# Kernel tuning notes

Hardware: AMD Instinct MI355X
Metric: run time of the kernel (lower is better)

The kernel has to match this reference:

```python
import jax, jax.numpy as jnp
import numpy as np

# static config (matches init_kwargs)
B, HID, NH, D = 1, 1024, 16, 64
T, Hh, W = 8, 32, 32
TT, TH, TW = 2, 8, 8            # tile sizes (numel 128)
WT, WH, WW = 6 // TT, 16 // TH, 16 // TW  # window in tiles: 3,2,2
NTT, NTH, NTW = T // TT, Hh // TH, W // TW  # 4,4,4
NTILE = NTT * NTH * NTW          # 64
TILE = TT * TH * TW              # 128
WK = WT * WH * WW                # 12 kv tiles per q tile
S = T * Hh * W


def _dim_window(nt, w):
    left = w // 2
    right = w // 2 + (w % 2) - 1
    center = jnp.clip(jnp.arange(nt), left, nt - 1 - right)
    return center[:, None] - left + jnp.arange(w)  # [nt, w]


def _kv_tile_idx():
    kt = _dim_window(NTT, WT)  # [NTT, WT]
    kh = _dim_window(NTH, WH)  # [NTH, WH]
    kw = _dim_window(NTW, WW)  # [NTW, WW]
    idx = (kt[:, None, None, :, None, None] * (NTH * NTW)
           + kh[None, :, None, None, :, None] * NTW
           + kw[None, None, :, None, None, :])
    return idx.reshape(NTILE, WK)


def _to_tiles(x, nh):
    # [B, S, nh*D] -> [B, nh, NTILE, TILE, D]; seq laid out (ntt tt nth th ntw tw)
    x = x.reshape(B, NTT, TT, NTH, TH, NTW, TW, nh, D)
    x = x.transpose(0, 7, 1, 3, 5, 2, 4, 6, 8)
    return x.reshape(B, nh, NTILE, TILE, D)


def _from_tiles(o):
    # [B, NH, NTILE, TILE, D] -> [B, S, NH*D]
    o = o.reshape(B, NH, NTT, NTH, NTW, TT, TH, TW, D)
    o = o.transpose(0, 2, 5, 3, 6, 4, 7, 1, 8)
    return o.reshape(B, S, NH * D)


def setup_inputs() -> dict:
    key = jax.random.key(0)
    ks = jax.random.split(key, 5)
    sc = 1.0 / np.sqrt(HID)
    return {
        'hidden_states': jax.random.normal(ks[0], (B, S, HID), jnp.float32),
        'wq': jax.random.normal(ks[1], (HID, NH * D), jnp.float32) * sc,
        'wk': jax.random.normal(ks[2], (HID, NH * D), jnp.float32) * sc,
        'wv': jax.random.normal(ks[3], (HID, NH * D), jnp.float32) * sc,
        'wo': jax.random.normal(ks[4], (NH * D, HID), jnp.float32) * sc,
    }


def reference(hidden_states, wq, wk, wv, wo):
    kv_idx = _kv_tile_idx()  # [NTILE, WK]
    q = _to_tiles(hidden_states @ wq, NH)  # [B,NH,NTILE,TILE,D]
    k = _to_tiles(hidden_states @ wk, NH)
    v = _to_tiles(hidden_states @ wv, NH)
    # gather each query tile's exact kv window (mask fully satisfied by construction)
    kg = k[:, :, kv_idx].reshape(B, NH, NTILE, WK * TILE, D)
    vg = v[:, :, kv_idx].reshape(B, NH, NTILE, WK * TILE, D)
    scores = jnp.einsum('bhnqd,bhnkd->bhnqk', q, kg) * (1.0 / np.sqrt(D))
    p = jax.nn.softmax(scores, axis=-1)
    o = jnp.einsum('bhnqk,bhnkd->bhnqd', p, vg)
    return _from_tiles(o) @ wo
```

## Files before the change

kernel.cpp:

```cpp
#include <hip/hip_runtime.h>
#include <hip/hip_bf16.h>
#include <math.h>

typedef __attribute__((ext_vector_type(8))) short          short8;
typedef __attribute__((ext_vector_type(8))) unsigned short u16x8;
typedef __attribute__((ext_vector_type(2))) unsigned int   u32x2;
typedef __attribute__((ext_vector_type(4))) float          f32x4;

#define MFMA_BF16(a, b, c) __builtin_amdgcn_mfma_f32_16x16x32_bf16((a), (b), (c), 0, 0, 0)

#define GLOAD_LDS16(gp, lp)                                        \
  __builtin_amdgcn_global_load_lds(                                \
      (const __attribute__((address_space(1))) void*)(gp),         \
      (__attribute__((address_space(3))) void*)(lp), 16, 0, 0)


__device__ __forceinline__ unsigned short f2bf(float f) {
  union { float f; unsigned int u; } v; v.f = f;
  unsigned int r = v.u + 0x7fffu + ((v.u >> 16) & 1u);
  return (unsigned short)(r >> 16);
}
__device__ __forceinline__ unsigned int pack2bf(float a, float b) {
  unsigned int r;
  asm("v_cvt_pk_bf16_f32 %0, %1, %2" : "=v"(r) : "v"(a), "v"(b));
  return r;
}

__device__ __forceinline__ int row_to_seq(int r) {
  int tile = r >> 7, pos = r & 127;
  int ntt = tile >> 4, nth = (tile >> 2) & 3, ntw = tile & 3;
  int tt  = pos >> 6,  th  = (pos >> 3) & 7,  tw  = pos & 7;
  return ((ntt * 2 + tt) << 10) | ((nth * 8 + th) << 5) | (ntw * 8 + tw);
}

__global__ __launch_bounds__(256) void permute_hs(const float* __restrict__ in,
                                                  unsigned short* __restrict__ out) {
  int cid = blockIdx.x * 256 + threadIdx.x;
  int r = cid >> 7, c = (cid & 127) * 8;
  int s = row_to_seq(r);
  const float* f = in + (size_t)s * 1024 + c;
  u16x8 v;
#pragma unroll
  for (int j = 0; j < 8; ++j) v[j] = f2bf(f[j]);
  *(u16x8*)(out + (size_t)r * 1024 + c) = v;
}

__global__ __launch_bounds__(256) void transpose_w(const float* __restrict__ w0,
                                                   const float* __restrict__ w1,
                                                   const float* __restrict__ w2,
                                                   const float* __restrict__ w3,
                                                   unsigned short* __restrict__ out) {
  __shared__ unsigned short Lt[64 * 68];
  int m = blockIdx.y;
  const float* W = (m == 0) ? w0 : (m == 1) ? w1 : (m == 2) ? w2 : w3;
  unsigned short* O = out + (size_t)m * 1048576;
  int k0 = (blockIdx.x >> 4) * 64, n0 = (blockIdx.x & 15) * 64;
  int tid = threadIdx.x;
#pragma unroll
  for (int i = 0; i < 2; ++i) {
    int cid = i * 256 + tid;
    int kr = cid >> 3, c = cid & 7;
    const float* f = W + (size_t)(k0 + kr) * 1024 + n0 + c * 8;
#pragma unroll
    for (int j = 0; j < 8; ++j) Lt[(c * 8 + j) * 68 + kr] = f2bf(f[j]);
  }
  __syncthreads();
#pragma unroll
  for (int i = 0; i < 2; ++i) {
    int cid = i * 256 + tid;
    int nr = cid >> 3, c = cid & 7;
    u16x8 v;
#pragma unroll
    for (int j = 0; j < 8; ++j) v[j] = Lt[nr * 68 + c * 8 + j];
    *(u16x8*)(O + (size_t)(n0 + nr) * 1024 + k0 + c * 8) = v;
  }
}

template <int SCATTER, int OUT_F32>
__device__ __forceinline__ void gemm_bt_body(const unsigned short* __restrict__ A,
                                             const unsigned short* __restrict__ Bt,
                                             void* __restrict__ Cv,
                                             int row0, int col0, float scale) {
  __shared__ unsigned short As[128 * 64];
  __shared__ unsigned short Bs[128 * 64];
  const int tid  = threadIdx.x;
  const int lane = tid & 63, w = tid >> 6;
  const int quad = lane >> 4, lm = lane & 15;
  const int wr = (w >> 1) * 64, wc = (w & 1) * 64;
  f32x4 acc[4][4] = {};
  for (int kt = 0; kt < 16; ++kt) {
    const int k0 = kt * 64;
    __syncthreads();
#pragma unroll
    for (int i = 0; i < 4; ++i) {
      int cid = i * 256 + tid;
      int r = cid >> 3, c = cid & 7;
      int cg = c ^ (r & 7);
      int base = (i * 256 + (tid & 192)) * 8;
      GLOAD_LDS16(A  + (size_t)(row0 + r) * 1024 + k0 + cg * 8, As + base);
      GLOAD_LDS16(Bt + (size_t)(col0 + r) * 1024 + k0 + cg * 8, Bs + base);
    }
    __syncthreads();
#pragma unroll
    for (int kh = 0; kh < 2; ++kh) {
      short8 af[4], bf[4];
#pragma unroll
      for (int t = 0; t < 4; ++t) {
        int ca = (kh * 4 + quad) ^ (lm & 7);
        af[t] = *(const short8*)(As + (wr + t * 16 + lm) * 64 + ca * 8);
        bf[t] = *(const short8*)(Bs + (wc + t * 16 + lm) * 64 + ca * 8);
      }
#pragma unroll
      for (int rt = 0; rt < 4; ++rt)
#pragma unroll
        for (int ct = 0; ct < 4; ++ct)
          acc[rt][ct] = MFMA_BF16(af[rt], bf[ct], acc[rt][ct]);
    }
  }
#pragma unroll
  for (int rt = 0; rt < 4; ++rt)
#pragma unroll
    for (int ct = 0; ct < 4; ++ct)
#pragma unroll
      for (int g = 0; g < 4; ++g) {
        int R  = row0 + wr + rt * 16 + quad * 4 + g;
        int Cc = col0 + wc + ct * 16 + lm;
        int Rs = SCATTER ? row_to_seq(R) : R;
        float vv = acc[rt][ct][g] * scale;
        if (OUT_F32) ((float*)Cv)[(size_t)Rs * 1024 + Cc] = vv;
        else ((unsigned short*)Cv)[(size_t)Rs * 1024 + Cc] = f2bf(vv);
      }
}

__global__ __launch_bounds__(256) void gemm_qkv(const unsigned short* __restrict__ A,
                                                const unsigned short* __restrict__ Wt,
                                                unsigned short* __restrict__ QKV) {
  float scale = (blockIdx.z == 0) ? 0.18033688011112042f : 1.0f;
  gemm_bt_body<0, 0>(A, Wt + (size_t)blockIdx.z * 1048576,
                     QKV + (size_t)blockIdx.z * 8388608,
                     blockIdx.y * 128, blockIdx.x * 128, scale);
}

__global__ __launch_bounds__(256) void gemm_out(const unsigned short* __restrict__ A,
                                                const unsigned short* __restrict__ Wt,
                                                float* __restrict__ Cout) {
  gemm_bt_body<1, 1>(A, Wt, Cout, blockIdx.y * 128, blockIdx.x * 128, 1.0f);
}

__global__ __launch_bounds__(256) void transpose_v(const unsigned short* __restrict__ V,
                                                   unsigned short* __restrict__ Vt) {
  __shared__ unsigned short Lt[64 * 136];
  int kt = blockIdx.x, h = blockIdx.y, tid = threadIdx.x;
#pragma unroll
  for (int i = 0; i < 4; ++i) {
    int cid = i * 256 + tid;
    int r = cid >> 3, c = cid & 7;
    u16x8 v = *(const u16x8*)(V + (size_t)(kt * 128 + r) * 1024 + h * 64 + c * 8);
#pragma unroll
    for (int j = 0; j < 8; ++j) Lt[(c * 8 + j) * 136 + r] = v[j];
  }
  __syncthreads();
#pragma unroll
  for (int i = 0; i < 4; ++i) {
    int cid = i * 256 + tid;
    int d = cid >> 4, c = cid & 15;
    u16x8 v = *(const u16x8*)(Lt + d * 136 + c * 8);
    *(u16x8*)(Vt + (size_t)(h * 64 + d) * 8192 + kt * 128 + c * 8) = v;
  }
}

__global__ __launch_bounds__(512, 4) void attn(const unsigned short* __restrict__ Q,
                                               const unsigned short* __restrict__ K,
                                               const unsigned short* __restrict__ Vt,
                                               unsigned short* __restrict__ O) {
  __shared__ unsigned short Ks[128 * 64];
  __shared__ unsigned short Vs[64 * 128];
  __shared__ unsigned short Pb[8 * 16 * 64];

  const int tid  = threadIdx.x;
  const int lane = tid & 63, w = tid >> 6;
  const int quad = lane >> 4, lm = lane & 15;
  unsigned short* Pbw = Pb + w * 1024;

  const int h = blockIdx.x >> 6, qt = blockIdx.x & 63;
  const int ntt = qt >> 4, nth = (qt >> 2) & 3, ntw = qt & 3;
  const int kt0 = min(max(ntt, 1), 2) - 1;
  const int kh0 = min(max(nth, 1), 3) - 1;
  const int kw0 = min(max(ntw, 1), 3) - 1;

  const int cid1 = 512 + tid;
  const int rK0 = tid  >> 3, cgK0 = (tid  & 7) ^ (rK0 & 7);
  const int rK1 = cid1 >> 3, cgK1 = (cid1 & 7) ^ (rK1 & 7);
  const unsigned koff0 = rK0 * 1024 + h * 64 + cgK0 * 8;
  const unsigned koff1 = rK1 * 1024 + h * 64 + cgK1 * 8;
  const int dV0 = tid  >> 4, cgV0 = (tid  & 15) ^ (dV0 & 7);
  const int dV1 = cid1 >> 4, cgV1 = (cid1 & 15) ^ (dV1 & 7);
  const unsigned voff0 = (h * 64 + dV0) * 8192 + cgV0 * 8;
  const unsigned voff1 = (h * 64 + dV1) * 8192 + cgV1 * 8;
  const unsigned ldsD0 = (tid & 448) * 8;
  const unsigned ldsD1 = (512 + (tid & 448)) * 8;

  short8 bq[2];
#pragma unroll
  for (int kh = 0; kh < 2; ++kh)
    bq[kh] = *(const short8*)(Q + (size_t)(qt * 128 + w * 16 + lm) * 1024
                                + h * 64 + kh * 32 + quad * 8);

  short8 ones8;
#pragma unroll
  for (int j = 0; j < 8; ++j) ones8[j] = (short)0x3F80;

  f32x4 o_acc[4] = {};
  f32x4 l_acc = {};

  {
    const unsigned k0 = (unsigned)(kt0 * 16 + kh0 * 4 + kw0) << 17;
    GLOAD_LDS16(K + koff0 + k0, Ks + ldsD0);
    GLOAD_LDS16(K + koff1 + k0, Ks + ldsD1);
  }
  __syncthreads();

  for (int it = 0; it < 12; ++it) {
    const int tt2 = it >> 2, hh2 = (it >> 1) & 1, ww2 = it & 1;
    const int kvt = (kt0 + tt2) * 16 + (kh0 + hh2) * 4 + (kw0 + ww2);

    {
      const unsigned v0 = (unsigned)kvt << 7;
      GLOAD_LDS16(Vt + voff0 + v0, Vs + ldsD0);
      GLOAD_LDS16(Vt + voff1 + v0, Vs + ldsD1);
    }

    f32x4 sa[8] = {};
#pragma unroll
    for (int kh = 0; kh < 2; ++kh) {
      short8 ak[8];
#pragma unroll
      for (int rt = 0; rt < 8; ++rt)
        ak[rt] = *(const short8*)(Ks + (rt * 16 + lm) * 64 + (((kh * 4 + quad) ^ (lm & 7)) * 8));
      __builtin_amdgcn_s_setprio(1);
#pragma unroll
      for (int rt = 0; rt < 8; ++rt)
        sa[rt] = MFMA_BF16(ak[rt], bq[kh], sa[rt]);
      __builtin_amdgcn_s_setprio(0);
    }

    u32x2 pk[8];
#pragma unroll
    for (int rt = 0; rt < 8; ++rt) {
      pk[rt][0] = pack2bf(exp2f(sa[rt][0]), exp2f(sa[rt][1]));
      pk[rt][1] = pack2bf(exp2f(sa[rt][2]), exp2f(sa[rt][3]));
    }

    __syncthreads();

    if (it < 11) {
      const int jt = it + 1;
      const int t2 = jt >> 2, h2 = (jt >> 1) & 1, w2 = jt & 1;
      const unsigned kn = (unsigned)((kt0 + t2) * 16 + (kh0 + h2) * 4 + (kw0 + w2)) << 17;
      GLOAD_LDS16(K + koff0 + kn, Ks + ldsD0);
      GLOAD_LDS16(K + koff1 + kn, Ks + ldsD1);
    }

#pragma unroll
    for (int half = 0; half < 2; ++half) {
#pragma unroll
      for (int rt4 = 0; rt4 < 4; ++rt4) {
        *(u32x2*)(Pbw + lm * 64 + (((rt4 * 2 + (quad >> 1)) ^ (lm & 7)) * 8) + (quad & 1) * 4)
            = pk[half * 4 + rt4];
      }
#pragma unroll
      for (int ks2 = 0; ks2 < 2; ++ks2) {
        short8 ap = *(const short8*)(Pbw + lm * 64 + (((ks2 * 4 + quad) ^ (lm & 7)) * 8));
        const int ks = half * 2 + ks2;
        __builtin_amdgcn_s_setprio(1);
        l_acc = MFMA_BF16(ap, ones8, l_acc);
        __builtin_amdgcn_s_setprio(0);
#pragma unroll
        for (int nt = 0; nt < 4; ++nt) {
          short8 bv = *(const short8*)(Vs + (nt * 16 + lm) * 128 + (((ks * 4 + quad) ^ (lm & 7)) * 8));
          __builtin_amdgcn_s_setprio(1);
          o_acc[nt] = MFMA_BF16(ap, bv, o_acc[nt]);
          __builtin_amdgcn_s_setprio(0);
        }
      }
    }

    __syncthreads();
  }

#pragma unroll
  for (int g = 0; g < 4; ++g) {
    float inv = 1.0f / l_acc[g];
#pragma unroll
    for (int nt = 0; nt < 4; ++nt) {
      int R = qt * 128 + w * 16 + quad * 4 + g;
      O[(size_t)R * 1024 + h * 64 + nt * 16 + lm] = f2bf(o_acc[nt][g] * inv);
    }
  }
}

extern "C" void kernel_launch(void* const* d_in, const int* in_sizes, int n_in,
                              void* d_out, int out_size, void* d_ws, size_t ws_size,
                              hipStream_t stream) {
  const float* hs = (const float*)d_in[0];
  const float* wq = (const float*)d_in[1];
  const float* wk = (const float*)d_in[2];
  const float* wv = (const float*)d_in[3];
  const float* wo = (const float*)d_in[4];
  float* out = (float*)d_out;

  const size_t NEL = 8388608;
  unsigned short* ws  = (unsigned short*)d_ws;
  unsigned short* HSt = ws;
  unsigned short* Qb  = ws + 1 * NEL;
  unsigned short* Kb  = ws + 2 * NEL;
  unsigned short* Vb  = ws + 3 * NEL;
  unsigned short* Vtb = ws + 4 * NEL;
  unsigned short* Ot  = ws + 5 * NEL;
  unsigned short* Wt  = ws + 6 * NEL;
  if (ws_size < (6 * NEL + 4 * 1048576) * sizeof(unsigned short)) return;

  permute_hs<<<4096, 256, 0, stream>>>(hs, HSt);
  transpose_w<<<dim3(256, 4), 256, 0, stream>>>(wq, wk, wv, wo, Wt);
  gemm_qkv<<<dim3(8, 64, 3), 256, 0, stream>>>(HSt, Wt, Qb);
  transpose_v<<<dim3(64, 16), 256, 0, stream>>>(Vb, Vtb);
  attn<<<1024, 512, 0, stream>>>(Qb, Kb, Vtb, Ot);
  gemm_out<<<dim3(8, 64, 1), 256, 0, stream>>>(Ot, Wt + 3 * 1048576, out);
  (void)in_sizes; (void)n_in; (void)out_size;
}
```

Before: 284.0 us.

## Double-buffer K and V tiles in LDS and batch V fragment loads

Allocates two LDS buffers each for K and V so the next KV tile's K and V are fetched asynchronously while the current tile is computed. This removes one barrier per iteration and stops V from being loaded in the same iteration it is consumed. It also hoists the four V fragment reads ahead of their MFMAs so they issue as a group. The larger LDS footprint may lower the number of resident blocks per CU.

```diff
diff --git a/kernel.cpp b/kernel.cpp
--- a/kernel.cpp
+++ b/kernel.cpp
@@ -173,8 +173,8 @@
                                                const unsigned short* __restrict__ K,
                                                const unsigned short* __restrict__ Vt,
                                                unsigned short* __restrict__ O) {
-  __shared__ unsigned short Ks[128 * 64];
-  __shared__ unsigned short Vs[64 * 128];
+  __shared__ unsigned short Ks[2][128 * 64];
+  __shared__ unsigned short Vs[2][64 * 128];
   __shared__ unsigned short Pb[8 * 16 * 64];
 
   const int tid  = threadIdx.x;
@@ -214,20 +214,31 @@
   f32x4 l_acc = {};
 
   {
-    const unsigned k0 = (unsigned)(kt0 * 16 + kh0 * 4 + kw0) << 17;
-    GLOAD_LDS16(K + koff0 + k0, Ks + ldsD0);
-    GLOAD_LDS16(K + koff1 + k0, Ks + ldsD1);
+    const int kvt0 = kt0 * 16 + kh0 * 4 + kw0;
+    const unsigned k0 = (unsigned)kvt0 << 17;
+    const unsigned v0 = (unsigned)kvt0 << 7;
+    GLOAD_LDS16(K  + koff0 + k0, Ks[0] + ldsD0);
+    GLOAD_LDS16(K  + koff1 + k0, Ks[0] + ldsD1);
+    GLOAD_LDS16(Vt + voff0 + v0, Vs[0] + ldsD0);
+    GLOAD_LDS16(Vt + voff1 + v0, Vs[0] + ldsD1);
   }
   __syncthreads();
 
   for (int it = 0; it < 12; ++it) {
-    const int tt2 = it >> 2, hh2 = (it >> 1) & 1, ww2 = it & 1;
-    const int kvt = (kt0 + tt2) * 16 + (kh0 + hh2) * 4 + (kw0 + ww2);
-
-    {
-      const unsigned v0 = (unsigned)kvt << 7;
-      GLOAD_LDS16(Vt + voff0 + v0, Vs + ldsD0);
-      GLOAD_LDS16(Vt + voff1 + v0, Vs + ldsD1);
+    const int p = it & 1;
+    const unsigned short* Ksp = Ks[p];
+    const unsigned short* Vsp = Vs[p];
+
+    if (it < 11) {
+      const int jt = it + 1;
+      const int t2 = jt >> 2, h2 = (jt >> 1) & 1, w2 = jt & 1;
+      const int kvn = (kt0 + t2) * 16 + (kh0 + h2) * 4 + (kw0 + w2);
+      const unsigned kn = (unsigned)kvn << 17;
+      const unsigned vn = (unsigned)kvn << 7;
+      GLOAD_LDS16(K  + koff0 + kn, Ks[1 - p] + ldsD0);
+      GLOAD_LDS16(K  + koff1 + kn, Ks[1 - p] + ldsD1);
+      GLOAD_LDS16(Vt + voff0 + vn, Vs[1 - p] + ldsD0);
+      GLOAD_LDS16(Vt + voff1 + vn, Vs[1 - p] + ldsD1);
     }
 
     f32x4 sa[8] = {};
@@ -236,7 +247,7 @@
       short8 ak[8];
 #pragma unroll
       for (int rt = 0; rt < 8; ++rt)
-        ak[rt] = *(const short8*)(Ks + (rt * 16 + lm) * 64 + (((kh * 4 + quad) ^ (lm & 7)) * 8));
+        ak[rt] = *(const short8*)(Ksp + (rt * 16 + lm) * 64 + (((kh * 4 + quad) ^ (lm & 7)) * 8));
       __builtin_amdgcn_s_setprio(1);
 #pragma unroll
       for (int rt = 0; rt < 8; ++rt)
@@ -249,16 +260,6 @@
     for (int rt = 0; rt < 8; ++rt) {
       pk[rt][0] = pack2bf(exp2f(sa[rt][0]), exp2f(sa[rt][1]));
       pk[rt][1] = pack2bf(exp2f(sa[rt][2]), exp2f(sa[rt][3]));
-    }
-
-    __syncthreads();
-
-    if (it < 11) {
-      const int jt = it + 1;
-      const int t2 = jt >> 2, h2 = (jt >> 1) & 1, w2 = jt & 1;
-      const unsigned kn = (unsigned)((kt0 + t2) * 16 + (kh0 + h2) * 4 + (kw0 + w2)) << 17;
-      GLOAD_LDS16(K + koff0 + kn, Ks + ldsD0);
-      GLOAD_LDS16(K + koff1 + kn, Ks + ldsD1);
     }
 
 #pragma unroll
@@ -272,16 +273,16 @@
       for (int ks2 = 0; ks2 < 2; ++ks2) {
         short8 ap = *(const short8*)(Pbw + lm * 64 + (((ks2 * 4 + quad) ^ (lm & 7)) * 8));
         const int ks = half * 2 + ks2;
+        short8 bv[4];
+#pragma unroll
+        for (int nt = 0; nt < 4; ++nt)
+          bv[nt] = *(const short8*)(Vsp + (nt * 16 + lm) * 128 + (((ks * 4 + quad) ^ (lm & 7)) * 8));
         __builtin_amdgcn_s_setprio(1);
         l_acc = MFMA_BF16(ap, ones8, l_acc);
+#pragma unroll
+        for (int nt = 0; nt < 4; ++nt)
+          o_acc[nt] = MFMA_BF16(ap, bv[nt], o_acc[nt]);
         __builtin_amdgcn_s_setprio(0);
-#pragma unroll
-        for (int nt = 0; nt < 4; ++nt) {
-          short8 bv = *(const short8*)(Vs + (nt * 16 + lm) * 128 + (((ks * 4 + quad) ^ (lm & 7)) * 8));
-          __builtin_amdgcn_s_setprio(1);
-          o_acc[nt] = MFMA_BF16(ap, bv, o_acc[nt]);
-          __builtin_amdgcn_s_setprio(0);
-        }
       }
     }
 
```

New measurement: 283.2 us. Within noise of the previous version (-0.3%).
